# Kernel tuning notes

Hardware: AMD Instinct MI355X
Metric: run time of the kernel (lower is better)

The kernel has to match this reference:

```python
import jax, jax.numpy as jnp
import numpy as np

DIM = 256
HEADS = 8
DIM_HEAD = 32
INNER = HEADS * DIM_HEAD
K_NEIGHBORS = 16
TEMPERATURE = 1.0
SCALE = DIM_HEAD ** (-0.5)
BATCH = 512
N_FEATURES = 32


def setup_inputs() -> dict:
    key = jax.random.key(0)
    ks = jax.random.split(key, 6)
    s = 0.02
    return {
        "x": jax.random.normal(ks[0], (BATCH, N_FEATURES, DIM), dtype=jnp.float32),
        "W_qkv": jax.random.normal(ks[1], (DIM, 3 * INNER), dtype=jnp.float32) * s,
        "W_out": jax.random.normal(ks[2], (INNER, DIM), dtype=jnp.float32) * s,
        "b_out": jnp.zeros((DIM,), dtype=jnp.float32),
        "W_repr": jax.random.normal(ks[3], (DIM, DIM), dtype=jnp.float32) * s,
        "b_repr": jnp.zeros((DIM,), dtype=jnp.float32),
    }


def reference(x, W_qkv, W_out, b_out, W_repr, b_repr):
    B, n, d = x.shape
    # A. sample representations: mean over features + linear proj
    reprs = jnp.mean(x, axis=1) @ W_repr + b_repr  # [B, dim]
    # B. kNN graph via cosine similarity
    normed = reprs / jnp.linalg.norm(reprs, axis=-1, keepdims=True)
    sim_mat = (normed @ normed.T) / TEMPERATURE  # [B, B]
    k_actual = min(K_NEIGHBORS + 1, B)
    _, knn_idx = jax.lax.top_k(sim_mat, k_actual)  # [B, k+1]
    # C. attention mask: 0 for self+neighbors, -inf elsewhere
    neg_inf = jnp.float32(-jnp.inf)
    mask = jnp.full((B, B), neg_inf, dtype=jnp.float32)
    mask = mask.at[jnp.arange(B)[:, None], knn_idx].set(0.0)  # [B, B]
    # D. masked cross-sample attention (vectorized over all features/heads)
    qkv = x @ W_qkv  # [B, n, 3*inner]
    q, k, v = jnp.split(qkv, 3, axis=-1)
    def to_bhnd(t):
        return t.reshape(B, n, HEADS, DIM_HEAD).transpose(0, 2, 1, 3)  # b h n d
    q, k, v = to_bhnd(q), to_bhnd(k), to_bhnd(v)
    # per-feature cross-sample scores: [n, b, h, B]
    sim = jnp.einsum('bhnd,Bhnd->nbhB', q, k) * SCALE
    sim = sim + mask[None, :, None, :]
    attn = jax.nn.softmax(sim, axis=-1)
    out = jnp.einsum('nbhB,Bhnd->bnhd', attn, v)  # [b, n, h, d]
    out = out.reshape(B, n, INNER)
    return out @ W_out + b_out
```

## Files before the change

kernel.cpp:

```cpp
#include <hip/hip_runtime.h>
#include <math.h>

#define DIMX 256
#define NFEAT 32
#define BATCH 512
#define HEADS 8
#define DHEAD 32
#define KNN 17
#define QKV_W 768
#define SCALE_F 0.17677669529663687f

typedef unsigned int uint;
typedef unsigned short ushort_t;
typedef __attribute__((ext_vector_type(8))) short short8_t;
typedef __attribute__((ext_vector_type(4))) float float4_t;

__device__ inline float bf_lo(uint u) { return __uint_as_float(u << 16); }
__device__ inline float bf_hi(uint u) { return __uint_as_float(u & 0xffff0000u); }
__device__ inline ushort_t f2bf(float f) {
  uint u = __float_as_uint(f);
  return (ushort_t)((u + 0x7fffu + ((u >> 16) & 1u)) >> 16);
}
__device__ inline void gload16(const ushort_t* g, ushort_t* l) {
  __builtin_amdgcn_global_load_lds(
      (const __attribute__((address_space(1))) void*)g,
      (__attribute__((address_space(3))) void*)l, 16, 0, 0);
}

__global__ void repr_kernel(const float* __restrict__ x, const float* __restrict__ W_repr,
                            const float* __restrict__ b_repr, float* __restrict__ normed,
                            ushort_t* __restrict__ xbf) {
  int b = blockIdx.x, t = threadIdx.x;
  __shared__ float mean_s[DIMX];
  __shared__ float red[DIMX];
  float s = 0.f;
#pragma unroll
  for (int n = 0; n < NFEAT; ++n) {
    float v = x[(size_t)(b*NFEAT+n)*DIMX + t];
    s += v;
    xbf[(size_t)(b*NFEAT+n)*DIMX + t] = f2bf(v);
  }
  mean_s[t] = s * (1.0f/NFEAT);
  __syncthreads();
  float acc = b_repr[t];
  for (int d = 0; d < DIMX; ++d) acc += mean_s[d] * W_repr[d*DIMX + t];
  red[t] = acc*acc;
  __syncthreads();
  for (int off = 128; off > 0; off >>= 1) {
    if (t < off) red[t] += red[t+off];
    __syncthreads();
  }
  normed[b*DIMX + t] = acc / sqrtf(red[0]);
}

__global__ __launch_bounds__(256, 4) void sim_gemm(const float* __restrict__ normed,
                                                   float* __restrict__ sims) {
  __shared__ float As[32][68];
  __shared__ float Bs[32][68];
  int t = threadIdx.x;
  int i0 = blockIdx.x * 32, j0 = blockIdx.y * 32;
  int tx = t & 15, ty = t >> 4;
  float acc00 = 0.f, acc01 = 0.f, acc10 = 0.f, acc11 = 0.f;
  for (int k0 = 0; k0 < DIMX; k0 += 64) {
#pragma unroll
    for (int c = t; c < 512; c += 256) {
      int r = c >> 4, cc = (c & 15) * 4;
      *(float4*)&As[r][cc] = *(const float4*)&normed[(size_t)(i0 + r)*DIMX + k0 + cc];
      *(float4*)&Bs[r][cc] = *(const float4*)&normed[(size_t)(j0 + r)*DIMX + k0 + cc];
    }
    __syncthreads();
#pragma unroll 16
    for (int kk = 0; kk < 64; ++kk) {
      float a0 = As[ty*2][kk],   a1 = As[ty*2+1][kk];
      float b0 = Bs[tx*2][kk],   b1 = Bs[tx*2+1][kk];
      acc00 += a0*b0; acc01 += a0*b1; acc10 += a1*b0; acc11 += a1*b1;
    }
    __syncthreads();
  }
  sims[(size_t)(i0+ty*2  )*BATCH + j0+tx*2  ] = acc00;
  sims[(size_t)(i0+ty*2  )*BATCH + j0+tx*2+1] = acc01;
  sims[(size_t)(i0+ty*2+1)*BATCH + j0+tx*2  ] = acc10;
  sims[(size_t)(i0+ty*2+1)*BATCH + j0+tx*2+1] = acc11;
}

__global__ __launch_bounds__(256, 8) void topk_rank(const float* __restrict__ sims,
                                                    int* __restrict__ knn) {
  int i = blockIdx.x, t = threadIdx.x;
  __shared__ float row[BATCH];
  row[t]       = sims[(size_t)i*BATCH + t];
  row[t + 256] = sims[(size_t)i*BATCH + t + 256];
  __syncthreads();
  float v1 = row[t], v2 = row[t + 256];
  int i1 = t, i2 = t + 256;
  int r1 = 0, r2 = 0;
  const float4* r4 = (const float4*)row;
#pragma unroll 8
  for (int c = 0; c < BATCH/4; ++c) {
    float4 q = r4[c];
    int base = c * 4;
    r1 += (q.x > v1 || (q.x == v1 && base+0 < i1));
    r1 += (q.y > v1 || (q.y == v1 && base+1 < i1));
    r1 += (q.z > v1 || (q.z == v1 && base+2 < i1));
    r1 += (q.w > v1 || (q.w == v1 && base+3 < i1));
    r2 += (q.x > v2 || (q.x == v2 && base+0 < i2));
    r2 += (q.y > v2 || (q.y == v2 && base+1 < i2));
    r2 += (q.z > v2 || (q.z == v2 && base+2 < i2));
    r2 += (q.w > v2 || (q.w == v2 && base+3 < i2));
  }
  if (r1 < KNN) knn[i*32 + r1] = i1;
  if (r2 < KNN) knn[i*32 + r2] = i2;
}

__global__ __launch_bounds__(256, 4) void prep_kernel(
    const float* __restrict__ Wq, const float* __restrict__ Wo,
    ushort_t* __restrict__ wqT, ushort_t* __restrict__ woT) {
  int bid = blockIdx.x, t = threadIdx.x;
  const float* W; ushort_t* WT; int NN, tx, ty;
  if (bid < 48) { W = Wq; WT = wqT; NN = QKV_W; tx = bid % 12; ty = bid / 12; }
  else { int b2 = bid - 48; W = Wo; WT = woT; NN = DIMX; tx = b2 % 4; ty = b2 / 4; }
  __shared__ float tile[64][65];
#pragma unroll
  for (int i = 0; i < 4; ++i) {
    int c = t + 256*i;
    int r = c >> 4, c4 = (c & 15) * 4;
    *(float4*)&tile[r][c4] = *(const float4*)&W[(size_t)(ty*64 + r)*NN + tx*64 + c4];
  }
  __syncthreads();
  int rr = t >> 2, cc0 = (t & 3) * 16;
  uint ow[8];
#pragma unroll
  for (int k = 0; k < 8; ++k)
    ow[k] = (uint)f2bf(tile[cc0 + 2*k][rr]) | ((uint)f2bf(tile[cc0 + 2*k + 1][rr]) << 16);
  uint4 o0 = {ow[0], ow[1], ow[2], ow[3]};
  uint4 o1 = {ow[4], ow[5], ow[6], ow[7]};
  size_t obase = (size_t)(tx*64 + rr)*DIMX + ty*64 + cc0;
  *(uint4*)&WT[obase]     = o0;
  *(uint4*)&WT[obase + 8] = o1;
}

template<bool OUTF32>
__global__ __launch_bounds__(256, 2) void mfma_gemm(
    const ushort_t* __restrict__ A, const ushort_t* __restrict__ Bt,
    void* __restrict__ Cout, const float* __restrict__ bias, int M, int N, int K) {
  __shared__ ushort_t As[2][128][64];
  __shared__ ushort_t Bs[2][128][64];
  int t = threadIdx.x, l = t & 63, w = t >> 6;
  int wr = w >> 1, wc = w & 1;
  int row0 = blockIdx.x * 128, col0 = blockIdx.y * 128;
  int srcRow = l >> 3;
  int srcCol = (l & 7) * 8;
  float4_t acc[4][4] = {};
  int nkt = K >> 6;
#pragma unroll
  for (int i = 0; i < 4; ++i) {
    int ar = w*32 + i*8;
    gload16(&A [(size_t)(row0+ar+srcRow)*K + srcCol], &As[0][ar][0]);
    gload16(&Bt[(size_t)(col0+ar+srcRow)*K + srcCol], &Bs[0][ar][0]);
  }
  __syncthreads();
  int cur = 0;
  for (int kt = 0; kt < nkt; ++kt) {
    if (kt + 1 < nkt) {
      int k1 = (kt + 1) << 6;
#pragma unroll
      for (int i = 0; i < 4; ++i) {
        int ar = w*32 + i*8;
        gload16(&A [(size_t)(row0+ar+srcRow)*K + k1 + srcCol], &As[cur^1][ar][0]);
        gload16(&Bt[(size_t)(col0+ar+srcRow)*K + k1 + srcCol], &Bs[cur^1][ar][0]);
      }
    }
#pragma unroll
    for (int ks = 0; ks < 2; ++ks) {
      int kk = ks*32 + (l >> 4)*8;
      short8_t a[4], b[4];
#pragma unroll
      for (int m = 0; m < 4; ++m) a[m] = *(short8_t*)&As[cur][wr*64 + m*16 + (l & 15)][kk];
#pragma unroll
      for (int n = 0; n < 4; ++n) b[n] = *(short8_t*)&Bs[cur][wc*64 + n*16 + (l & 15)][kk];
#pragma unroll
      for (int m = 0; m < 4; ++m)
#pragma unroll
        for (int n = 0; n < 4; ++n)
          acc[m][n] = __builtin_amdgcn_mfma_f32_16x16x32_bf16(a[m], b[n], acc[m][n], 0, 0, 0);
    }
    __syncthreads();
    cur ^= 1;
  }
  int crow = (l >> 4) * 4, ccol = l & 15;
#pragma unroll
  for (int m = 0; m < 4; ++m)
#pragma unroll
    for (int n = 0; n < 4; ++n) {
      int col = col0 + wc*64 + n*16 + ccol;
#pragma unroll
      for (int r = 0; r < 4; ++r) {
        int row = row0 + wr*64 + m*16 + crow + r;
        if (OUTF32) ((float*)Cout)[(size_t)row*N + col] = acc[m][n][r] + bias[col];
        else        ((ushort_t*)Cout)[(size_t)row*N + col] = f2bf(acc[m][n][r]);
      }
    }
}

#define NF_BLK 8
__global__ __launch_bounds__(256, 8) void attn_kernel(
    const ushort_t* __restrict__ qkv, const int* __restrict__ knn,
    ushort_t* __restrict__ attn_out) {
  int b = blockIdx.x, g = blockIdx.y, t = threadIdx.x;
  int n0 = g * NF_BLK;
  __shared__ float sc_s[2][KNN][HEADS];
  __shared__ int idxs[KNN];
  if (t < KNN) idxs[t] = knn[b*32 + t];
  __syncthreads();

  for (int np = 0; np < NF_BLK; np += 2) {
    int n = n0 + np;
    for (int job = t; job < 2*KNN*HEADS; job += 256) {
      int f = (job >= KNN*HEADS) ? 1 : 0;
      int r = job - f*KNN*HEADS;
      int j = r >> 3, h = r & 7;
      const uint4* qp = (const uint4*)&qkv[(size_t)(b*NFEAT + n + f)*QKV_W + h*DHEAD];
      const uint4* kp = (const uint4*)&qkv[(size_t)(idxs[j]*NFEAT + n + f)*QKV_W + 256 + h*DHEAD];
      float s = 0.f;
#pragma unroll
      for (int i = 0; i < 4; ++i) {
        uint4 qv = qp[i], kv = kp[i];
        s += bf_lo(qv.x)*bf_lo(kv.x) + bf_hi(qv.x)*bf_hi(kv.x)
           + bf_lo(qv.y)*bf_lo(kv.y) + bf_hi(qv.y)*bf_hi(kv.y)
           + bf_lo(qv.z)*bf_lo(kv.z) + bf_hi(qv.z)*bf_hi(kv.z)
           + bf_lo(qv.w)*bf_lo(kv.w) + bf_hi(qv.w)*bf_hi(kv.w);
      }
      sc_s[f][j][h] = s * SCALE_F;
    }
    __syncthreads();
    {
      int f = t >> 7, p = t & 127, h = p >> 4;
      float m = -INFINITY;
#pragma unroll
      for (int j = 0; j < KNN; ++j) m = fmaxf(m, sc_s[f][j][h]);
      float sum = 0.f;
#pragma unroll
      for (int j = 0; j < KNN; ++j) sum += __expf(sc_s[f][j][h] - m);
      float inv = 1.0f / sum;
      float alo = 0.f, ahi = 0.f;
#pragma unroll
      for (int j = 0; j < KNN; ++j) {
        float pw = __expf(sc_s[f][j][h] - m);
        uint wv = *(const uint*)&qkv[(size_t)(idxs[j]*NFEAT + n + f)*QKV_W + 512 + p*2];
        alo += pw * bf_lo(wv);
        ahi += pw * bf_hi(wv);
      }
      *(uint*)&attn_out[(size_t)(b*NFEAT + n + f)*DIMX + p*2] =
          (uint)f2bf(alo * inv) | ((uint)f2bf(ahi * inv) << 16);
    }
    __syncthreads();
  }
}

extern "C" void kernel_launch(void* const* d_in, const int* in_sizes, int n_in,
                              void* d_out, int out_size, void* d_ws, size_t ws_size,
                              hipStream_t stream) {
  const float* x      = (const float*)d_in[0];
  const float* W_qkv  = (const float*)d_in[1];
  const float* W_out  = (const float*)d_in[2];
  const float* b_out  = (const float*)d_in[3];
  const float* W_repr = (const float*)d_in[4];
  const float* b_repr = (const float*)d_in[5];
  float* out = (float*)d_out;

  ushort_t* qkv      = (ushort_t*)d_ws;
  ushort_t* xbf      = qkv + (size_t)16384*QKV_W;
  ushort_t* wqT      = xbf + (size_t)16384*DIMX;
  ushort_t* woT      = wqT + (size_t)QKV_W*DIMX;
  ushort_t* attn_out = woT + (size_t)DIMX*DIMX;
  float*    normed   = (float*)(attn_out + (size_t)16384*DIMX);
  float*    sims     = normed + (size_t)BATCH*DIMX;
  int*      knn      = (int*)(sims + (size_t)BATCH*BATCH);

  repr_kernel<<<BATCH, 256, 0, stream>>>(x, W_repr, b_repr, normed, xbf);
  sim_gemm<<<dim3(BATCH/32, BATCH/32), 256, 0, stream>>>(normed, sims);
  topk_rank<<<BATCH, 256, 0, stream>>>(sims, knn);
  prep_kernel<<<64, 256, 0, stream>>>(W_qkv, W_out, wqT, woT);
  mfma_gemm<false><<<dim3(16384/128, QKV_W/128), 256, 0, stream>>>(
      xbf, wqT, qkv, nullptr, 16384, QKV_W, DIMX);
  attn_kernel<<<dim3(BATCH, NFEAT/NF_BLK), 256, 0, stream>>>(qkv, knn, attn_out);
  mfma_gemm<true><<<dim3(16384/128, DIMX/128), 256, 0, stream>>>(
      attn_out, woT, out, b_out, 16384, DIMX, DIMX);
}
```

Measured before the change: 103.8 us.

## Merge independent kernels into combined launches and use dot2/exp2 in attention

Puts the repr and weight-prep work into one launch, and the QKV GEMM and similarity GEMM into another, using block-index dispatch. This cuts the launch count from seven to five and lets independent work run side by side. The attention kernel now uses bf16 dot2 instructions for the QK scores and exp2 with a log2-folded scale. It also precomputes neighbor row offsets and caches the exponentials in registers instead of recomputing them. The trade-off is more register pressure in the attention kernel and shared-memory reuse across the different roles in the merged kernels.

```diff
diff --git a/kernel.cpp b/kernel.cpp
--- a/kernel.cpp
+++ b/kernel.cpp
@@ -8,7 +8,7 @@
 #define DHEAD 32
 #define KNN 17
 #define QKV_W 768
-#define SCALE_F 0.17677669529663687f
+#define SCALE_L2 0.25503486f
 
 typedef unsigned int uint;
 typedef unsigned short ushort_t;
@@ -21,66 +21,200 @@
   uint u = __float_as_uint(f);
   return (ushort_t)((u + 0x7fffu + ((u >> 16) & 1u)) >> 16);
 }
+
+#if defined(__has_builtin)
+#if __has_builtin(__builtin_amdgcn_fdot2_f32_bf16)
+#define HAVE_DOT2 1
+#endif
+#if __has_builtin(__builtin_amdgcn_exp2f)
+#define EXP2(x) __builtin_amdgcn_exp2f(x)
+#endif
+#endif
+#ifndef EXP2
+#define EXP2(x) exp2f(x)
+#endif
+
+#ifdef HAVE_DOT2
+typedef __attribute__((ext_vector_type(2))) __bf16 bf16x2_t;
+__device__ inline float dot2bf(uint a, uint b, float c) {
+  return __builtin_amdgcn_fdot2_f32_bf16(
+      __builtin_bit_cast(bf16x2_t, a), __builtin_bit_cast(bf16x2_t, b), c, false);
+}
+#else
+__device__ inline float dot2bf(uint a, uint b, float c) {
+  return c + bf_lo(a)*bf_lo(b) + bf_hi(a)*bf_hi(b);
+}
+#endif
+
 __device__ inline void gload16(const ushort_t* g, ushort_t* l) {
   __builtin_amdgcn_global_load_lds(
       (const __attribute__((address_space(1))) void*)g,
       (__attribute__((address_space(3))) void*)l, 16, 0, 0);
 }
 
-__global__ void repr_kernel(const float* __restrict__ x, const float* __restrict__ W_repr,
-                            const float* __restrict__ b_repr, float* __restrict__ normed,
-                            ushort_t* __restrict__ xbf) {
-  int b = blockIdx.x, t = threadIdx.x;
-  __shared__ float mean_s[DIMX];
-  __shared__ float red[DIMX];
-  float s = 0.f;
-#pragma unroll
-  for (int n = 0; n < NFEAT; ++n) {
-    float v = x[(size_t)(b*NFEAT+n)*DIMX + t];
-    s += v;
-    xbf[(size_t)(b*NFEAT+n)*DIMX + t] = f2bf(v);
-  }
-  mean_s[t] = s * (1.0f/NFEAT);
+__global__ __launch_bounds__(256, 2) void repr_prep_kernel(
+    const float* __restrict__ x, const float* __restrict__ W_repr,
+    const float* __restrict__ b_repr, const float* __restrict__ Wq,
+    const float* __restrict__ Wo, float* __restrict__ normed,
+    ushort_t* __restrict__ xbf, ushort_t* __restrict__ wqT, ushort_t* __restrict__ woT) {
+  __shared__ float smem[64*65];
+  int bid = blockIdx.x, t = threadIdx.x;
+  if (bid < BATCH) {
+    float* mean_s = smem;
+    float* red = smem + 256;
+    int b = bid;
+    float s = 0.f;
+#pragma unroll
+    for (int n = 0; n < NFEAT; ++n) {
+      float v = x[(size_t)(b*NFEAT+n)*DIMX + t];
+      s += v;
+      xbf[(size_t)(b*NFEAT+n)*DIMX + t] = f2bf(v);
+    }
+    mean_s[t] = s * (1.0f/NFEAT);
+    __syncthreads();
+    float acc = b_repr[t];
+    for (int d = 0; d < DIMX; ++d) acc += mean_s[d] * W_repr[d*DIMX + t];
+    red[t] = acc*acc;
+    __syncthreads();
+    for (int off = 128; off > 0; off >>= 1) {
+      if (t < off) red[t] += red[t+off];
+      __syncthreads();
+    }
+    normed[b*DIMX + t] = acc / sqrtf(red[0]);
+  } else {
+    int pb = bid - BATCH;
+    const float* W; ushort_t* WT; int NN, tx, ty;
+    if (pb < 48) { W = Wq; WT = wqT; NN = QKV_W; tx = pb % 12; ty = pb / 12; }
+    else { int b2 = pb - 48; W = Wo; WT = woT; NN = DIMX; tx = b2 % 4; ty = b2 / 4; }
+    float (*tile)[65] = (float(*)[65])smem;
+#pragma unroll
+    for (int i = 0; i < 4; ++i) {
+      int c = t + 256*i;
+      int r = c >> 4, c4 = (c & 15) * 4;
+      *(float4*)&tile[r][c4] = *(const float4*)&W[(size_t)(ty*64 + r)*NN + tx*64 + c4];
+    }
+    __syncthreads();
+    int rr = t >> 2, cc0 = (t & 3) * 16;
+    uint ow[8];
+#pragma unroll
+    for (int k = 0; k < 8; ++k)
+      ow[k] = (uint)f2bf(tile[cc0 + 2*k][rr]) | ((uint)f2bf(tile[cc0 + 2*k + 1][rr]) << 16);
+    uint4 o0 = {ow[0], ow[1], ow[2], ow[3]};
+    uint4 o1 = {ow[4], ow[5], ow[6], ow[7]};
+    size_t obase = (size_t)(tx*64 + rr)*DIMX + ty*64 + cc0;
+    *(uint4*)&WT[obase]     = o0;
+    *(uint4*)&WT[obase + 8] = o1;
+  }
+}
+
+template<bool OUTF32>
+__device__ __forceinline__ void gemm_body(
+    ushort_t (&As)[2][128][64], ushort_t (&Bs)[2][128][64],
+    const ushort_t* __restrict__ A, const ushort_t* __restrict__ Bt,
+    void* __restrict__ Cout, const float* __restrict__ bias,
+    int M, int N, int K, int row0, int col0) {
+  int t = threadIdx.x, l = t & 63, w = t >> 6;
+  int wr = w >> 1, wc = w & 1;
+  int srcRow = l >> 3, srcCol = (l & 7) * 8;
+  float4_t acc[4][4] = {};
+  int nkt = K >> 6;
+#pragma unroll
+  for (int i = 0; i < 4; ++i) {
+    int ar = w*32 + i*8;
+    gload16(&A [(size_t)(row0+ar+srcRow)*K + srcCol], &As[0][ar][0]);
+    gload16(&Bt[(size_t)(col0+ar+srcRow)*K + srcCol], &Bs[0][ar][0]);
+  }
   __syncthreads();
-  float acc = b_repr[t];
-  for (int d = 0; d < DIMX; ++d) acc += mean_s[d] * W_repr[d*DIMX + t];
-  red[t] = acc*acc;
-  __syncthreads();
-  for (int off = 128; off > 0; off >>= 1) {
-    if (t < off) red[t] += red[t+off];
-    __syncthreads();
-  }
-  normed[b*DIMX + t] = acc / sqrtf(red[0]);
-}
-
-__global__ __launch_bounds__(256, 4) void sim_gemm(const float* __restrict__ normed,
-                                                   float* __restrict__ sims) {
-  __shared__ float As[32][68];
-  __shared__ float Bs[32][68];
-  int t = threadIdx.x;
-  int i0 = blockIdx.x * 32, j0 = blockIdx.y * 32;
-  int tx = t & 15, ty = t >> 4;
-  float acc00 = 0.f, acc01 = 0.f, acc10 = 0.f, acc11 = 0.f;
-  for (int k0 = 0; k0 < DIMX; k0 += 64) {
-#pragma unroll
-    for (int c = t; c < 512; c += 256) {
-      int r = c >> 4, cc = (c & 15) * 4;
-      *(float4*)&As[r][cc] = *(const float4*)&normed[(size_t)(i0 + r)*DIMX + k0 + cc];
-      *(float4*)&Bs[r][cc] = *(const float4*)&normed[(size_t)(j0 + r)*DIMX + k0 + cc];
-    }
-    __syncthreads();
+  int cur = 0;
+  for (int kt = 0; kt < nkt; ++kt) {
+    if (kt + 1 < nkt) {
+      int k1 = (kt + 1) << 6;
+#pragma unroll
+      for (int i = 0; i < 4; ++i) {
+        int ar = w*32 + i*8;
+        gload16(&A [(size_t)(row0+ar+srcRow)*K + k1 + srcCol], &As[cur^1][ar][0]);
+        gload16(&Bt[(size_t)(col0+ar+srcRow)*K + k1 + srcCol], &Bs[cur^1][ar][0]);
+      }
+    }
+#pragma unroll
+    for (int ks = 0; ks < 2; ++ks) {
+      int kk = ks*32 + (l >> 4)*8;
+      short8_t a[4], b[4];
+#pragma unroll
+      for (int m = 0; m < 4; ++m) a[m] = *(short8_t*)&As[cur][wr*64 + m*16 + (l & 15)][kk];
+#pragma unroll
+      for (int n = 0; n < 4; ++n) b[n] = *(short8_t*)&Bs[cur][wc*64 + n*16 + (l & 15)][kk];
+#pragma unroll
+      for (int m = 0; m < 4; ++m)
+#pragma unroll
+        for (int n = 0; n < 4; ++n)
+          acc[m][n] = __builtin_amdgcn_mfma_f32_16x16x32_bf16(a[m], b[n], acc[m][n], 0, 0, 0);
+    }
+    __syncthreads();
+    cur ^= 1;
+  }
+  int crow = (l >> 4) * 4, ccol = l & 15;
+#pragma unroll
+  for (int m = 0; m < 4; ++m)
+#pragma unroll
+    for (int n = 0; n < 4; ++n) {
+      int col = col0 + wc*64 + n*16 + ccol;
+#pragma unroll
+      for (int r = 0; r < 4; ++r) {
+        int row = row0 + wr*64 + m*16 + crow + r;
+        if (OUTF32) ((float*)Cout)[(size_t)row*N + col] = acc[m][n][r] + bias[col];
+        else        ((ushort_t*)Cout)[(size_t)row*N + col] = f2bf(acc[m][n][r]);
+      }
+    }
+}
+
+template<bool OUTF32>
+__global__ __launch_bounds__(256, 2) void mfma_gemm(
+    const ushort_t* __restrict__ A, const ushort_t* __restrict__ Bt,
+    void* __restrict__ Cout, const float* __restrict__ bias, int M, int N, int K) {
+  __shared__ ushort_t As[2][128][64];
+  __shared__ ushort_t Bs[2][128][64];
+  gemm_body<OUTF32>(As, Bs, A, Bt, Cout, bias, M, N, K, blockIdx.x*128, blockIdx.y*128);
+}
+
+__global__ __launch_bounds__(256, 2) void simqkv_kernel(
+    const ushort_t* __restrict__ xbf, const ushort_t* __restrict__ wqT,
+    ushort_t* __restrict__ qkv, const float* __restrict__ normed,
+    float* __restrict__ sims) {
+  __shared__ ushort_t As[2][128][64];
+  __shared__ ushort_t Bs[2][128][64];
+  int bid = blockIdx.x, t = threadIdx.x;
+  if (bid < 768) {
+    gemm_body<false>(As, Bs, xbf, wqT, qkv, nullptr, 16384, QKV_W, DIMX,
+                     (bid & 127) * 128, (bid >> 7) * 128);
+  } else {
+    int sid = bid - 768;
+    int i0 = (sid & 15) * 32, j0 = (sid >> 4) * 32;
+    float (*sA)[68] = (float(*)[68])(&As[0][0][0]);
+    float (*sB)[68] = (float(*)[68])(&Bs[0][0][0]);
+    int tx = t & 15, ty = t >> 4;
+    float acc00 = 0.f, acc01 = 0.f, acc10 = 0.f, acc11 = 0.f;
+    for (int k0 = 0; k0 < DIMX; k0 += 64) {
+#pragma unroll
+      for (int c = t; c < 512; c += 256) {
+        int r = c >> 4, cc = (c & 15) * 4;
+        *(float4*)&sA[r][cc] = *(const float4*)&normed[(size_t)(i0 + r)*DIMX + k0 + cc];
+        *(float4*)&sB[r][cc] = *(const float4*)&normed[(size_t)(j0 + r)*DIMX + k0 + cc];
+      }
+      __syncthreads();
 #pragma unroll 16
-    for (int kk = 0; kk < 64; ++kk) {
-      float a0 = As[ty*2][kk],   a1 = As[ty*2+1][kk];
-      float b0 = Bs[tx*2][kk],   b1 = Bs[tx*2+1][kk];
-      acc00 += a0*b0; acc01 += a0*b1; acc10 += a1*b0; acc11 += a1*b1;
-    }
-    __syncthreads();
-  }
-  sims[(size_t)(i0+ty*2  )*BATCH + j0+tx*2  ] = acc00;
-  sims[(size_t)(i0+ty*2  )*BATCH + j0+tx*2+1] = acc01;
-  sims[(size_t)(i0+ty*2+1)*BATCH + j0+tx*2  ] = acc10;
-  sims[(size_t)(i0+ty*2+1)*BATCH + j0+tx*2+1] = acc11;
+      for (int kk = 0; kk < 64; ++kk) {
+        float a0 = sA[ty*2][kk],   a1 = sA[ty*2+1][kk];
+        float b0 = sB[tx*2][kk],   b1 = sB[tx*2+1][kk];
+        acc00 += a0*b0; acc01 += a0*b1; acc10 += a1*b0; acc11 += a1*b1;
+      }
+      __syncthreads();
+    }
+    sims[(size_t)(i0+ty*2  )*BATCH + j0+tx*2  ] = acc00;
+    sims[(size_t)(i0+ty*2  )*BATCH + j0+tx*2+1] = acc01;
+    sims[(size_t)(i0+ty*2+1)*BATCH + j0+tx*2  ] = acc10;
+    sims[(size_t)(i0+ty*2+1)*BATCH + j0+tx*2+1] = acc11;
+  }
 }
 
 __global__ __launch_bounds__(256, 8) void topk_rank(const float* __restrict__ sims,
@@ -111,96 +245,6 @@
   if (r2 < KNN) knn[i*32 + r2] = i2;
 }
 
-__global__ __launch_bounds__(256, 4) void prep_kernel(
-    const float* __restrict__ Wq, const float* __restrict__ Wo,
-    ushort_t* __restrict__ wqT, ushort_t* __restrict__ woT) {
-  int bid = blockIdx.x, t = threadIdx.x;
-  const float* W; ushort_t* WT; int NN, tx, ty;
-  if (bid < 48) { W = Wq; WT = wqT; NN = QKV_W; tx = bid % 12; ty = bid / 12; }
-  else { int b2 = bid - 48; W = Wo; WT = woT; NN = DIMX; tx = b2 % 4; ty = b2 / 4; }
-  __shared__ float tile[64][65];
-#pragma unroll
-  for (int i = 0; i < 4; ++i) {
-    int c = t + 256*i;
-    int r = c >> 4, c4 = (c & 15) * 4;
-    *(float4*)&tile[r][c4] = *(const float4*)&W[(size_t)(ty*64 + r)*NN + tx*64 + c4];
-  }
-  __syncthreads();
-  int rr = t >> 2, cc0 = (t & 3) * 16;
-  uint ow[8];
-#pragma unroll
-  for (int k = 0; k < 8; ++k)
-    ow[k] = (uint)f2bf(tile[cc0 + 2*k][rr]) | ((uint)f2bf(tile[cc0 + 2*k + 1][rr]) << 16);
-  uint4 o0 = {ow[0], ow[1], ow[2], ow[3]};
-  uint4 o1 = {ow[4], ow[5], ow[6], ow[7]};
-  size_t obase = (size_t)(tx*64 + rr)*DIMX + ty*64 + cc0;
-  *(uint4*)&WT[obase]     = o0;
-  *(uint4*)&WT[obase + 8] = o1;
-}
-
-template<bool OUTF32>
-__global__ __launch_bounds__(256, 2) void mfma_gemm(
-    const ushort_t* __restrict__ A, const ushort_t* __restrict__ Bt,
-    void* __restrict__ Cout, const float* __restrict__ bias, int M, int N, int K) {
-  __shared__ ushort_t As[2][128][64];
-  __shared__ ushort_t Bs[2][128][64];
-  int t = threadIdx.x, l = t & 63, w = t >> 6;
-  int wr = w >> 1, wc = w & 1;
-  int row0 = blockIdx.x * 128, col0 = blockIdx.y * 128;
-  int srcRow = l >> 3;
-  int srcCol = (l & 7) * 8;
-  float4_t acc[4][4] = {};
-  int nkt = K >> 6;
-#pragma unroll
-  for (int i = 0; i < 4; ++i) {
-    int ar = w*32 + i*8;
-    gload16(&A [(size_t)(row0+ar+srcRow)*K + srcCol], &As[0][ar][0]);
-    gload16(&Bt[(size_t)(col0+ar+srcRow)*K + srcCol], &Bs[0][ar][0]);
-  }
-  __syncthreads();
-  int cur = 0;
-  for (int kt = 0; kt < nkt; ++kt) {
-    if (kt + 1 < nkt) {
-      int k1 = (kt + 1) << 6;
-#pragma unroll
-      for (int i = 0; i < 4; ++i) {
-        int ar = w*32 + i*8;
-        gload16(&A [(size_t)(row0+ar+srcRow)*K + k1 + srcCol], &As[cur^1][ar][0]);
-        gload16(&Bt[(size_t)(col0+ar+srcRow)*K + k1 + srcCol], &Bs[cur^1][ar][0]);
-      }
-    }
-#pragma unroll
-    for (int ks = 0; ks < 2; ++ks) {
-      int kk = ks*32 + (l >> 4)*8;
-      short8_t a[4], b[4];
-#pragma unroll
-      for (int m = 0; m < 4; ++m) a[m] = *(short8_t*)&As[cur][wr*64 + m*16 + (l & 15)][kk];
-#pragma unroll
-      for (int n = 0; n < 4; ++n) b[n] = *(short8_t*)&Bs[cur][wc*64 + n*16 + (l & 15)][kk];
-#pragma unroll
-      for (int m = 0; m < 4; ++m)
-#pragma unroll
-        for (int n = 0; n < 4; ++n)
-          acc[m][n] = __builtin_amdgcn_mfma_f32_16x16x32_bf16(a[m], b[n], acc[m][n], 0, 0, 0);
-    }
-    __syncthreads();
-    cur ^= 1;
-  }
-  int crow = (l >> 4) * 4, ccol = l & 15;
-#pragma unroll
-  for (int m = 0; m < 4; ++m)
-#pragma unroll
-    for (int n = 0; n < 4; ++n) {
-      int col = col0 + wc*64 + n*16 + ccol;
-#pragma unroll
-      for (int r = 0; r < 4; ++r) {
-        int row = row0 + wr*64 + m*16 + crow + r;
-        if (OUTF32) ((float*)Cout)[(size_t)row*N + col] = acc[m][n][r] + bias[col];
-        else        ((ushort_t*)Cout)[(size_t)row*N + col] = f2bf(acc[m][n][r]);
-      }
-    }
-}
-
 #define NF_BLK 8
 __global__ __launch_bounds__(256, 8) void attn_kernel(
     const ushort_t* __restrict__ qkv, const int* __restrict__ knn,
@@ -208,8 +252,8 @@
   int b = blockIdx.x, g = blockIdx.y, t = threadIdx.x;
   int n0 = g * NF_BLK;
   __shared__ float sc_s[2][KNN][HEADS];
-  __shared__ int idxs[KNN];
-  if (t < KNN) idxs[t] = knn[b*32 + t];
+  __shared__ int idxp[KNN];
+  if (t < KNN) idxp[t] = knn[b*32 + t] * (NFEAT*QKV_W);
   __syncthreads();
 
   for (int np = 0; np < NF_BLK; np += 2) {
@@ -219,35 +263,36 @@
       int r = job - f*KNN*HEADS;
       int j = r >> 3, h = r & 7;
       const uint4* qp = (const uint4*)&qkv[(size_t)(b*NFEAT + n + f)*QKV_W + h*DHEAD];
-      const uint4* kp = (const uint4*)&qkv[(size_t)(idxs[j]*NFEAT + n + f)*QKV_W + 256 + h*DHEAD];
-      float s = 0.f;
+      const uint4* kp = (const uint4*)&qkv[(size_t)(idxp[j] + (n + f)*QKV_W + 256 + h*DHEAD)];
+      float s0 = 0.f, s1 = 0.f;
 #pragma unroll
       for (int i = 0; i < 4; ++i) {
         uint4 qv = qp[i], kv = kp[i];
-        s += bf_lo(qv.x)*bf_lo(kv.x) + bf_hi(qv.x)*bf_hi(kv.x)
-           + bf_lo(qv.y)*bf_lo(kv.y) + bf_hi(qv.y)*bf_hi(kv.y)
-           + bf_lo(qv.z)*bf_lo(kv.z) + bf_hi(qv.z)*bf_hi(kv.z)
-           + bf_lo(qv.w)*bf_lo(kv.w) + bf_hi(qv.w)*bf_hi(kv.w);
-      }
-      sc_s[f][j][h] = s * SCALE_F;
+        s0 = dot2bf(kv.x, qv.x, s0); s1 = dot2bf(kv.y, qv.y, s1);
+        s0 = dot2bf(kv.z, qv.z, s0); s1 = dot2bf(kv.w, qv.w, s1);
+      }
+      sc_s[f][j][h] = (s0 + s1) * SCALE_L2;
     }
     __syncthreads();
     {
       int f = t >> 7, p = t & 127, h = p >> 4;
-      float m = -INFINITY;
-#pragma unroll
-      for (int j = 0; j < KNN; ++j) m = fmaxf(m, sc_s[f][j][h]);
+      float sv[KNN];
+#pragma unroll
+      for (int j = 0; j < KNN; ++j) sv[j] = sc_s[f][j][h];
+      float m = sv[0];
+#pragma unroll
+      for (int j = 1; j < KNN; ++j) m = fmaxf(m, sv[j]);
       float sum = 0.f;
 #pragma unroll
-      for (int j = 0; j < KNN; ++j) sum += __expf(sc_s[f][j][h] - m);
+      for (int j = 0; j < KNN; ++j) { sv[j] = EXP2(sv[j] - m); sum += sv[j]; }
       float inv = 1.0f / sum;
+      int voff = (n + f)*QKV_W + 512 + p*2;
       float alo = 0.f, ahi = 0.f;
 #pragma unroll
       for (int j = 0; j < KNN; ++j) {
-        float pw = __expf(sc_s[f][j][h] - m);
-        uint wv = *(const uint*)&qkv[(size_t)(idxs[j]*NFEAT + n + f)*QKV_W + 512 + p*2];
-        alo += pw * bf_lo(wv);
-        ahi += pw * bf_hi(wv);
+        uint wv = *(const uint*)&qkv[(size_t)(idxp[j] + voff)];
+        alo += sv[j] * bf_lo(wv);
+        ahi += sv[j] * bf_hi(wv);
       }
       *(uint*)&attn_out[(size_t)(b*NFEAT + n + f)*DIMX + p*2] =
           (uint)f2bf(alo * inv) | ((uint)f2bf(ahi * inv) << 16);
@@ -276,13 +321,11 @@
   float*    sims     = normed + (size_t)BATCH*DIMX;
   int*      knn      = (int*)(sims + (size_t)BATCH*BATCH);
 
-  repr_kernel<<<BATCH, 256, 0, stream>>>(x, W_repr, b_repr, normed, xbf);
-  sim_gemm<<<dim3(BATCH/32, BATCH/32), 256, 0, stream>>>(normed, sims);
+  repr_prep_kernel<<<BATCH + 64, 256, 0, stream>>>(
+      x, W_repr, b_repr, W_qkv, W_out, normed, xbf, wqT, woT);
+  simqkv_kernel<<<768 + 256, 256, 0, stream>>>(xbf, wqT, qkv, normed, sims);
   topk_rank<<<BATCH, 256, 0, stream>>>(sims, knn);
-  prep_kernel<<<64, 256, 0, stream>>>(W_qkv, W_out, wqT, woT);
-  mfma_gemm<false><<<dim3(16384/128, QKV_W/128), 256, 0, stream>>>(
-      xbf, wqT, qkv, nullptr, 16384, QKV_W, DIMX);
   attn_kernel<<<dim3(BATCH, NFEAT/NF_BLK), 256, 0, stream>>>(qkv, knn, attn_out);
-  mfma_gemm<true><<<dim3(16384/128, DIMX/128), 256, 0, stream>>>(
+  mfma_gemm<true><<<dim3(128, 2), 256, 0, stream>>>(
       attn_out, woT, out, b_out, 16384, DIMX, DIMX);
 }
```

After: 94.28 us. 1.1x faster.
